# Optimization experiments

Measured on AMD Instinct MI355X. Metric: run time of the kernel, lower is better.

The kernel has to match this reference:

```python
import jax, jax.numpy as jnp
import numpy as np

B, S, D, H, E, F = 32, 196, 768, 12, 8, 3072  # batch, seq, d_model, heads, experts, ffn
DH = D // H
EPS = 1e-5


def setup_inputs() -> dict:
    key = jax.random.key(0)
    ks = jax.random.split(key, 16)
    n = lambda k, shape, s=0.02: (jax.random.normal(k, shape, dtype=jnp.float32) * s)
    return {
        "q": jax.random.normal(ks[0], (B, S, D), dtype=jnp.float32),
        "k": jax.random.normal(ks[1], (B, S, D), dtype=jnp.float32),
        "v": jax.random.normal(ks[2], (B, S, D), dtype=jnp.float32),
        "Wq": n(ks[3], (D, D)), "bq": jnp.zeros((D,), jnp.float32),
        "Wk": n(ks[4], (D, D)), "bk": jnp.zeros((D,), jnp.float32),
        "Wv": n(ks[5], (D, D)), "bv": jnp.zeros((D,), jnp.float32),
        "Wo": n(ks[6], (D, D)), "bo": jnp.zeros((D,), jnp.float32),
        "ln1_g": jnp.ones((D,), jnp.float32), "ln1_b": jnp.zeros((D,), jnp.float32),
        "ln2_g": jnp.ones((D,), jnp.float32), "ln2_b": jnp.zeros((D,), jnp.float32),
        "Wg": n(ks[7], (D, E)), "bg": jnp.zeros((E,), jnp.float32),
        "W1": n(ks[8], (E, D, F)), "b1": jnp.zeros((E, F), jnp.float32),
        "W2": n(ks[9], (E, F, D)), "b2": jnp.zeros((E, D), jnp.float32),
    }


def _layernorm(x, g, b):
    mu = jnp.mean(x, axis=-1, keepdims=True)
    var = jnp.mean(jnp.square(x - mu), axis=-1, keepdims=True)
    return (x - mu) * jax.lax.rsqrt(var + EPS) * g + b


def reference(q, k, v, Wq, bq, Wk, bk, Wv, bv, Wo, bo,
              ln1_g, ln1_b, ln2_g, ln2_b, Wg, bg, W1, b1, W2, b2):
    # --- multi-head attention (batch_first, scaled dot product) ---
    qh = (q @ Wq + bq).reshape(B, S, H, DH)
    kh = (k @ Wk + bk).reshape(B, S, H, DH)
    vh = (v @ Wv + bv).reshape(B, S, H, DH)
    scores = jnp.einsum('bqhd,bkhd->bhqk', qh, kh) / np.float32(np.sqrt(DH))
    attn = jax.nn.softmax(scores, axis=-1)
    ctx = jnp.einsum('bhqk,bkhd->bqhd', attn, vh).reshape(B, S, D)
    attn_out = ctx @ Wo + bo

    # --- residual + LN 1 ---
    x = _layernorm(q + attn_out, ln1_g, ln1_b)

    # --- MoE: per-token soft gating over per-expert FFNs ---
    gates = jax.nn.softmax(x @ Wg + bg, axis=-1)                 # [B,S,E]
    h = jax.nn.gelu(jnp.einsum('bsd,edf->bsef', x, W1) + b1,
                    approximate=False)                            # [B,S,E,F]
    y = jnp.einsum('bsef,efd->bsed', h, W2) + b2                 # [B,S,E,D]
    moe_out = jnp.einsum('bse,bsed->bsd', gates, y)              # [B,S,D]

    # --- residual + LN 2 ---
    return _layernorm(x + moe_out, ln2_g, ln2_b)
```

## Files before the change

### kernel.cpp

```cpp
#include <hip/hip_runtime.h>
#include <cmath>

#define B_  32
#define S_  196
#define D_  768
#define H_  12
#define E_  8
#define F_  3072
#define DH_ 64
#define T_  (B_ * S_)

typedef unsigned short ushort_t;
typedef short   s16x8   __attribute__((ext_vector_type(8)));
typedef __bf16  bf16x8_t __attribute__((ext_vector_type(8)));
typedef float   f32x4   __attribute__((ext_vector_type(4)));

struct ABFrag {
    unsigned int r[4];
    __device__ operator s16x8()    const { return __builtin_bit_cast(s16x8, *this); }
    __device__ operator bf16x8_t() const { return __builtin_bit_cast(bf16x8_t, *this); }
};

__device__ __forceinline__ ushort_t f2bf(float f) {
    unsigned int x = __float_as_uint(f);
    return (ushort_t)((x + 0x7fffu + ((x >> 16) & 1u)) >> 16);
}

__device__ __forceinline__ void glds16(const void* g, void* l) {
    __builtin_amdgcn_global_load_lds((const __attribute__((address_space(1))) void*)g,
                                     (__attribute__((address_space(3))) void*)l,
                                     16, 0, 0);
}

__device__ __forceinline__ void atomAddF(float* p, float v) {
    __hip_atomic_fetch_add(p, v, __ATOMIC_RELAXED, __HIP_MEMORY_SCOPE_AGENT);
}

template<int EPI>
__global__ __launch_bounds__(256)
void gemm_bt(const ushort_t* __restrict__ A0, const ushort_t* __restrict__ A1,
             const ushort_t* __restrict__ A2, const ushort_t* __restrict__ Bt,
             const float* __restrict__ bias,
             float* __restrict__ C0, float* __restrict__ C1,
             float* __restrict__ C2,
             ushort_t* __restrict__ Cb0, ushort_t* __restrict__ Cb1,
             int M, int N, int K, int lda, int ldb,
             size_t strideB, int biasStride,
             const float* __restrict__ gates, int expertBase)
{
    __shared__ ushort_t Alds[128 * 32];
    __shared__ ushort_t Blds[128 * 32];

    const int tid = threadIdx.x;
    const int w  = tid >> 6, l = tid & 63;
    const int wr = w >> 1,  wc = w & 1;
    const int rg = l >> 4,  fr = l & 15;
    const int brow = blockIdx.y * 128;
    const int bcol = blockIdx.x * 128;
    const int z    = blockIdx.z;

    int e = 0, koff = 0;
    const ushort_t* A = A0;
    const ushort_t* Bp = Bt;
    if (EPI == 1) { e = z; Bp += (size_t)e * strideB; }
    if (EPI == 2) { e = z >> 1; koff = (z & 1) * K; A = e ? A1 : A0;
                    Bp += (size_t)e * strideB; }

    const int seg = (EPI == 3) ? (bcol / 768) : 0;
    if (EPI == 3) A = (seg == 0 ? A0 : seg == 1 ? A1 : A2);
    float* Cf = (EPI == 3) ? (seg == 0 ? C0 : seg == 1 ? C1 : C2) : C0;
    const int ldc   = (EPI == 3) ? 768 : N;
    const int ccol0 = (EPI == 3) ? (bcol - seg * 768) : bcol;

    const int srow = tid >> 2;
    const int scol = (tid & 3) << 3;
    const ushort_t* gA = A  + (size_t)(brow + srow) * lda + koff + scol;
    const ushort_t* gB = Bp + (size_t)(bcol + srow) * ldb + koff + scol;
    ushort_t* lA = &Alds[w * 512];
    ushort_t* lB = &Blds[w * 512];

    f32x4 acc[4][4] = {};
    const int aoff = (wr * 64 + fr) * 32 + rg * 8;
    const int boff = (wc * 64 + fr) * 32 + rg * 8;

    for (int k0 = 0; k0 < K; k0 += 32) {
        if (k0) __syncthreads();
        glds16(gA,                    lA);
        glds16(gA + (size_t)64 * lda, lA + 2048);
        glds16(gB,                    lB);
        glds16(gB + (size_t)64 * ldb, lB + 2048);
        gA += 32; gB += 32;
        __syncthreads();

        ABFrag af[4], bfr[4];
        #pragma unroll
        for (int m = 0; m < 4; ++m) af[m]  = *(const ABFrag*)&Alds[aoff + m * 512];
        #pragma unroll
        for (int n = 0; n < 4; ++n) bfr[n] = *(const ABFrag*)&Blds[boff + n * 512];
        #pragma unroll
        for (int m = 0; m < 4; ++m)
            #pragma unroll
            for (int n = 0; n < 4; ++n)
                acc[m][n] = __builtin_amdgcn_mfma_f32_16x16x32_bf16(
                                af[m], bfr[n], acc[m][n], 0, 0, 0);
    }

    #pragma unroll
    for (int m = 0; m < 4; ++m) {
        #pragma unroll
        for (int n = 0; n < 4; ++n) {
            const int cg   = bcol  + wc * 64 + n * 16 + fr;
            const int ocol = ccol0 + wc * 64 + n * 16 + fr;
            float bv;
            if (EPI == 1)      bv = bias[e * biasStride + cg];
            else if (EPI == 2) bv = (z & 1) ? 0.f : bias[e * biasStride + cg];
            else               bv = bias[cg];
            #pragma unroll
            for (int j = 0; j < 4; ++j) {
                const int row = brow + wr * 64 + m * 16 + rg * 4 + j;
                float vv = acc[m][n][j] + bv;
                if (EPI == 1) {
                    vv = 0.5f * vv * (1.0f + erff(vv * 0.70710678118654752f));
                    (e ? Cb1 : Cb0)[(size_t)row * N + ocol] = f2bf(vv);
                } else if (EPI == 2) {
                    atomAddF(&Cf[(size_t)row * ldc + ocol],
                             gates[(size_t)row * E_ + expertBase + e] * vv);
                } else {
                    Cf[(size_t)row * ldc + ocol] = vv;
                }
            }
        }
    }
}

__global__ __launch_bounds__(256)
void convert_bf16(const float* __restrict__ in, ushort_t* __restrict__ out)
{
    const int i = blockIdx.x * 256 + threadIdx.x;
    float4 v = ((const float4*)in)[i];
    ushort4 o;
    o.x = f2bf(v.x); o.y = f2bf(v.y); o.z = f2bf(v.z); o.w = f2bf(v.w);
    ((ushort4*)out)[i] = o;
}

__global__ __launch_bounds__(256)
void transpose_to_bf16(const float* __restrict__ in, ushort_t* __restrict__ out,
                       int R, int C, size_t inStride, size_t outStride)
{
    __shared__ float tile[64][65];
    in  += (size_t)blockIdx.z * inStride;
    out += (size_t)blockIdx.z * outStride;
    const int bc = blockIdx.x * 64;
    const int br = blockIdx.y * 64;
    const int lr = threadIdx.x >> 4;
    const int lc = (threadIdx.x & 15) << 2;
    #pragma unroll
    for (int i = 0; i < 64; i += 16) {
        float4 v = *(const float4*)&in[(size_t)(br + lr + i) * C + bc + lc];
        tile[lr + i][lc + 0] = v.x; tile[lr + i][lc + 1] = v.y;
        tile[lr + i][lc + 2] = v.z; tile[lr + i][lc + 3] = v.w;
    }
    __syncthreads();
    #pragma unroll
    for (int i = 0; i < 64; i += 16) {
        const int orow = lr + i;
        ushort4 o;
        o.x = f2bf(tile[lc + 0][orow]);
        o.y = f2bf(tile[lc + 1][orow]);
        o.z = f2bf(tile[lc + 2][orow]);
        o.w = f2bf(tile[lc + 3][orow]);
        *(ushort4*)&out[(size_t)(bc + orow) * R + br + lc] = o;
    }
}

#define KB_ 28
__global__ __launch_bounds__(256)
void attn_kernel(const float* __restrict__ qh, const float* __restrict__ kh,
                 const float* __restrict__ vh, float* __restrict__ ctx)
{
    __shared__ float Ks[S_ * DH_];
    const int bh = blockIdx.x;
    const int b  = bh / H_;
    const int h  = bh % H_;
    const int tid = threadIdx.x;

    for (int i = tid; i < S_ * 16; i += 256) {
        const int s = i >> 4, d4 = i & 15;
        ((float4*)Ks)[s * 16 + d4] =
            *(const float4*)&kh[((size_t)(b * S_ + s)) * D_ + h * DH_ + d4 * 4];
    }
    __syncthreads();
    if (tid >= S_) return;

    float qf[DH_];
    const float* qrow = qh + ((size_t)(b * S_ + tid)) * D_ + h * DH_;
    #pragma unroll
    for (int d = 0; d < DH_; d += 4) {
        float4 v4 = *(const float4*)(qrow + d);
        qf[d+0] = v4.x * 0.125f; qf[d+1] = v4.y * 0.125f;
        qf[d+2] = v4.z * 0.125f; qf[d+3] = v4.w * 0.125f;
    }

    float m = -1e30f, lsum = 0.f;
    float acc[DH_] = {};
    const float* vbase = vh + ((size_t)b * S_) * D_ + h * DH_;

    for (int kc = 0; kc < S_; kc += KB_) {
        float sc[KB_];
        #pragma unroll
        for (int kk = 0; kk < KB_; ++kk) {
            const float* kr = &Ks[(kc + kk) * DH_];
            float s0 = 0.f, s1 = 0.f, s2 = 0.f, s3 = 0.f;
            #pragma unroll
            for (int d = 0; d < DH_; d += 4) {
                s0 = fmaf(qf[d+0], kr[d+0], s0);
                s1 = fmaf(qf[d+1], kr[d+1], s1);
                s2 = fmaf(qf[d+2], kr[d+2], s2);
                s3 = fmaf(qf[d+3], kr[d+3], s3);
            }
            sc[kk] = (s0 + s1) + (s2 + s3);
        }
        float cmax = sc[0];
        #pragma unroll
        for (int kk = 1; kk < KB_; ++kk) cmax = fmaxf(cmax, sc[kk]);
        const float newm  = fmaxf(m, cmax);
        const float alpha = __expf(m - newm);
        lsum *= alpha;
        #pragma unroll
        for (int d = 0; d < DH_; ++d) acc[d] *= alpha;
        m = newm;
        #pragma unroll
        for (int kk = 0; kk < KB_; ++kk) {
            sc[kk] = __expf(sc[kk] - m);
            lsum  += sc[kk];
        }
        #pragma unroll
        for (int kk = 0; kk < KB_; ++kk) {
            const float p = sc[kk];
            const float* vr = vbase + (size_t)(kc + kk) * D_;
            #pragma unroll
            for (int d = 0; d < DH_; d += 4) {
                float4 v4 = *(const float4*)(vr + d);
                acc[d+0] = fmaf(p, v4.x, acc[d+0]);
                acc[d+1] = fmaf(p, v4.y, acc[d+1]);
                acc[d+2] = fmaf(p, v4.z, acc[d+2]);
                acc[d+3] = fmaf(p, v4.w, acc[d+3]);
            }
        }
    }
    const float inv = 1.f / lsum;
    float* crow = ctx + ((size_t)(b * S_ + tid)) * D_ + h * DH_;
    #pragma unroll
    for (int d = 0; d < DH_; ++d) crow[d] = acc[d] * inv;
}

__device__ __forceinline__ float block_sum(float v, float* red)
{
    __syncthreads();
    const int lane = threadIdx.x & 63;
    const int wid  = threadIdx.x >> 6;
    #pragma unroll
    for (int off = 32; off > 0; off >>= 1) v += __shfl_down(v, off);
    if (lane == 0) red[wid] = v;
    __syncthreads();
    return red[0] + red[1] + red[2] + red[3];
}

__global__ __launch_bounds__(256)
void ln_kernel(const float* __restrict__ a, const float* __restrict__ bres,
               const float* __restrict__ g, const float* __restrict__ beta,
               float* __restrict__ out, float* __restrict__ zt)
{
    __shared__ float red[4];
    const int t   = blockIdx.x;
    const int tid = threadIdx.x;
    const float* ar = a    + (size_t)t * D_;
    const float* br = bres + (size_t)t * D_;

    float vals[3];
    float s = 0.f;
    #pragma unroll
    for (int i = 0; i < 3; ++i) {
        const int d = tid + i * 256;
        const float x = ar[d] + br[d];
        vals[i] = x;
        s += x;
        if (zt) zt[(size_t)t * D_ + d] = 0.f;
    }
    s = block_sum(s, red);
    const float mu = s * (1.f / D_);
    float qv = 0.f;
    #pragma unroll
    for (int i = 0; i < 3; ++i) { const float dv = vals[i] - mu; qv += dv * dv; }
    qv = block_sum(qv, red);
    const float rstd = rsqrtf(qv * (1.f / D_) + 1e-5f);
    #pragma unroll
    for (int i = 0; i < 3; ++i) {
        const int d = tid + i * 256;
        out[(size_t)t * D_ + d] = (vals[i] - mu) * rstd * g[d] + beta[d];
    }
}

__global__ __launch_bounds__(256)
void gate_kernel(const float* __restrict__ x, const float* __restrict__ Wg,
                 const float* __restrict__ bg, float* __restrict__ gates)
{
    const int lane = threadIdx.x & 63;
    const int wid  = threadIdx.x >> 6;
    const int t = blockIdx.x * 4 + wid;
    const float* xr = x + (size_t)t * D_;

    float accv[E_];
    #pragma unroll
    for (int e = 0; e < E_; ++e) accv[e] = 0.f;
    for (int d = lane; d < D_; d += 64) {
        const float xv = xr[d];
        const float* wr = Wg + (size_t)d * E_;
        #pragma unroll
        for (int e = 0; e < E_; ++e) accv[e] = fmaf(xv, wr[e], accv[e]);
    }
    #pragma unroll
    for (int e = 0; e < E_; ++e) {
        #pragma unroll
        for (int off = 32; off > 0; off >>= 1)
            accv[e] += __shfl_down(accv[e], off);
    }
    if (lane == 0) {
        float mx = -1e30f;
        #pragma unroll
        for (int e = 0; e < E_; ++e) { accv[e] += bg[e]; mx = fmaxf(mx, accv[e]); }
        float lsum = 0.f;
        #pragma unroll
        for (int e = 0; e < E_; ++e) { const float p = expf(accv[e] - mx); accv[e] = p; lsum += p; }
        const float inv = 1.f / lsum;
        #pragma unroll
        for (int e = 0; e < E_; ++e) gates[(size_t)t * E_ + e] = accv[e] * inv;
    }
}

__global__ void concat3_kernel(const float* __restrict__ a, const float* __restrict__ b,
                               const float* __restrict__ c, float* __restrict__ o)
{
    const int i = blockIdx.x * 256 + threadIdx.x;
    if (i < 768)       o[i] = a[i];
    else if (i < 1536) o[i] = b[i - 768];
    else if (i < 2304) o[i] = c[i - 1536];
}

extern "C" void kernel_launch(void* const* d_in, const int* in_sizes, int n_in,
                              void* d_out, int out_size, void* d_ws, size_t ws_size,
                              hipStream_t stream)
{
    const float* q    = (const float*)d_in[0];
    const float* k    = (const float*)d_in[1];
    const float* v    = (const float*)d_in[2];
    const float* Wq   = (const float*)d_in[3];
    const float* bq   = (const float*)d_in[4];
    const float* Wk   = (const float*)d_in[5];
    const float* bk   = (const float*)d_in[6];
    const float* Wv   = (const float*)d_in[7];
    const float* bv   = (const float*)d_in[8];
    const float* Wo   = (const float*)d_in[9];
    const float* bo   = (const float*)d_in[10];
    const float* ln1g = (const float*)d_in[11];
    const float* ln1b = (const float*)d_in[12];
    const float* ln2g = (const float*)d_in[13];
    const float* ln2b = (const float*)d_in[14];
    const float* Wg   = (const float*)d_in[15];
    const float* bg   = (const float*)d_in[16];
    const float* W1   = (const float*)d_in[17];
    const float* b1   = (const float*)d_in[18];
    const float* W2   = (const float*)d_in[19];
    const float* b2   = (const float*)d_in[20];
    float* out = (float*)d_out;
    float* ws  = (float*)d_ws;

    const size_t TD = (size_t)T_ * D_;
    const size_t DD = (size_t)D_ * D_;
    const size_t DF = (size_t)D_ * F_;

    float* qh      = ws;
    float* x       = ws + TD;
    float* kh      = x;
    float* vh      = ws + 2 * TD;
    float* ctx     = ws + 3 * TD;
    float* moe     = ws + 4 * TD;
    ushort_t* hb0  = (ushort_t*)(ws + 2 * TD);
    ushort_t* hb1  = (ushort_t*)(ws + 5 * TD);
    ushort_t* xb   = (ushort_t*)qh;
    float* gates   = qh + TD / 2;
    float* attnout = qh;

    ushort_t* qb   = (ushort_t*)(ws + 5 * TD);
    ushort_t* kb   = qb + TD;
    ushort_t* vb   = kb + TD;
    ushort_t* ctxb = qb;

    ushort_t* wqkvt = (ushort_t*)(ws + 7 * TD);
    ushort_t* wot   = wqkvt + 3 * DD;
    float*    bcat  = (float*)(wot + DD);
    ushort_t* w1t   = (ushort_t*)(bcat + 2304);
    ushort_t* w2t   = w1t + 2 * DF;

    const dim3 blk(256);
    const int  cgrid = (int)(TD / 1024);

    concat3_kernel<<<dim3(9), blk, 0, stream>>>(bq, bk, bv, bcat);
    transpose_to_bf16<<<dim3(D_/64, D_/64), blk, 0, stream>>>(Wq, wqkvt,          D_, D_, 0, 0);
    transpose_to_bf16<<<dim3(D_/64, D_/64), blk, 0, stream>>>(Wk, wqkvt + DD,     D_, D_, 0, 0);
    transpose_to_bf16<<<dim3(D_/64, D_/64), blk, 0, stream>>>(Wv, wqkvt + 2 * DD, D_, D_, 0, 0);
    transpose_to_bf16<<<dim3(D_/64, D_/64), blk, 0, stream>>>(Wo, wot,            D_, D_, 0, 0);

    convert_bf16<<<cgrid, blk, 0, stream>>>(q, qb);
    convert_bf16<<<cgrid, blk, 0, stream>>>(k, kb);
    convert_bf16<<<cgrid, blk, 0, stream>>>(v, vb);
    gemm_bt<3><<<dim3(18, 49), blk, 0, stream>>>(qb, kb, vb, wqkvt, bcat,
                                                 qh, kh, vh, nullptr, nullptr,
                                                 T_, 2304, D_, D_, D_, 0, 0,
                                                 nullptr, 0);

    attn_kernel<<<dim3(B_ * H_), blk, 0, stream>>>(qh, kh, vh, ctx);

    convert_bf16<<<cgrid, blk, 0, stream>>>(ctx, ctxb);
    gemm_bt<0><<<dim3(6, 49), blk, 0, stream>>>(ctxb, nullptr, nullptr, wot, bo,
                                                attnout, nullptr, nullptr, nullptr, nullptr,
                                                T_, D_, D_, D_, D_, 0, 0, nullptr, 0);
    ln_kernel<<<dim3(T_), blk, 0, stream>>>(q, attnout, ln1g, ln1b, x, moe);

    gate_kernel<<<dim3(T_ / 4), blk, 0, stream>>>(x, Wg, bg, gates);
    convert_bf16<<<cgrid, blk, 0, stream>>>(x, xb);

    for (int g = 0; g < 4; ++g) {
        const int e0 = 2 * g;
        transpose_to_bf16<<<dim3(F_/64, D_/64, 2), blk, 0, stream>>>(
            W1 + (size_t)e0 * DF, w1t, D_, F_, DF, DF);
        transpose_to_bf16<<<dim3(D_/64, F_/64, 2), blk, 0, stream>>>(
            W2 + (size_t)e0 * DF, w2t, F_, D_, DF, DF);
        gemm_bt<1><<<dim3(24, 49, 2), blk, 0, stream>>>(
            xb, nullptr, nullptr, w1t, b1 + (size_t)e0 * F_,
            nullptr, nullptr, nullptr, hb0, hb1,
            T_, F_, D_, D_, D_, DF, F_, nullptr, 0);
        gemm_bt<2><<<dim3(6, 49, 4), blk, 0, stream>>>(
            hb0, hb1, nullptr, w2t, b2 + (size_t)e0 * D_,
            moe, nullptr, nullptr, nullptr, nullptr,
            T_, D_, F_ / 2, F_, F_, DF, D_, gates, e0);
    }

    ln_kernel<<<dim3(T_), blk, 0, stream>>>(x, moe, ln2g, ln2b, out, nullptr);
}
```

Before: 1.631 ms.

## Double GEMM K-tile with swizzled LDS, split attention over keys, fuse bf16 conversions

The GEMM now stages 64-wide K tiles with an XOR-swizzled LDS layout, which halves the number of barriers per tile and is meant to reduce bank conflicts. The exact erf GELU is replaced by a tanh-based approximation. Attention is split into two key halves across twice as many blocks, followed by a combine kernel that writes bf16 context directly. LayerNorm 1 also emits the bf16 copy of x, removing two conversion kernels. The costs are extra LDS use, an extra partial-results buffer, and slight numerical deviation from the tanh GELU.

```diff
diff --git a/kernel.cpp b/kernel.cpp
--- a/kernel.cpp
+++ b/kernel.cpp
@@ -9,6 +9,7 @@
 #define F_  3072
 #define DH_ 64
 #define T_  (B_ * S_)
+#define PR_ (B_ * H_ * S_)
 
 typedef unsigned short ushort_t;
 typedef short   s16x8   __attribute__((ext_vector_type(8)));
@@ -34,6 +35,12 @@
 
 __device__ __forceinline__ void atomAddF(float* p, float v) {
     __hip_atomic_fetch_add(p, v, __ATOMIC_RELAXED, __HIP_MEMORY_SCOPE_AGENT);
+}
+
+__device__ __forceinline__ float gelu_f(float x) {
+    const float y = 0.7978845608028654f * (x + 0.044715f * x * x * x);
+    const float t = __expf(fminf(2.f * y, 80.f));
+    return 0.5f * x * (1.f + (t - 1.f) / (t + 1.f));
 }
 
 template<int EPI>
@@ -48,8 +55,8 @@
              size_t strideB, int biasStride,
              const float* __restrict__ gates, int expertBase)
 {
-    __shared__ ushort_t Alds[128 * 32];
-    __shared__ ushort_t Blds[128 * 32];
+    __shared__ ushort_t Alds[128 * 64];
+    __shared__ ushort_t Blds[128 * 64];
 
     const int tid = threadIdx.x;
     const int w  = tid >> 6, l = tid & 63;
@@ -72,37 +79,44 @@
     const int ldc   = (EPI == 3) ? 768 : N;
     const int ccol0 = (EPI == 3) ? (bcol - seg * 768) : bcol;
 
-    const int srow = tid >> 2;
-    const int scol = (tid & 3) << 3;
+    const int srow = tid >> 3;
+    const int scol = ((tid & 7) << 3) ^ ((srow & 7) << 3);
     const ushort_t* gA = A  + (size_t)(brow + srow) * lda + koff + scol;
     const ushort_t* gB = Bp + (size_t)(bcol + srow) * ldb + koff + scol;
     ushort_t* lA = &Alds[w * 512];
     ushort_t* lB = &Blds[w * 512];
 
     f32x4 acc[4][4] = {};
-    const int aoff = (wr * 64 + fr) * 32 + rg * 8;
-    const int boff = (wc * 64 + fr) * 32 + rg * 8;
-
-    for (int k0 = 0; k0 < K; k0 += 32) {
+    const int arow0 = (wr * 64 + fr) * 64;
+    const int brow0 = (wc * 64 + fr) * 64;
+
+    for (int k0 = 0; k0 < K; k0 += 64) {
         if (k0) __syncthreads();
-        glds16(gA,                    lA);
-        glds16(gA + (size_t)64 * lda, lA + 2048);
-        glds16(gB,                    lB);
-        glds16(gB + (size_t)64 * ldb, lB + 2048);
-        gA += 32; gB += 32;
+        #pragma unroll
+        for (int s = 0; s < 4; ++s) {
+            glds16(gA + (size_t)(s * 32) * lda, lA + s * 2048);
+            glds16(gB + (size_t)(s * 32) * ldb, lB + s * 2048);
+        }
+        gA += 64; gB += 64;
         __syncthreads();
 
-        ABFrag af[4], bfr[4];
-        #pragma unroll
-        for (int m = 0; m < 4; ++m) af[m]  = *(const ABFrag*)&Alds[aoff + m * 512];
-        #pragma unroll
-        for (int n = 0; n < 4; ++n) bfr[n] = *(const ABFrag*)&Blds[boff + n * 512];
-        #pragma unroll
-        for (int m = 0; m < 4; ++m)
+        #pragma unroll
+        for (int kk = 0; kk < 2; ++kk) {
+            const int xk = (((kk << 2) | rg) ^ (fr & 7)) << 3;
+            ABFrag af[4], bfr[4];
+            #pragma unroll
+            for (int m = 0; m < 4; ++m)
+                af[m]  = *(const ABFrag*)&Alds[arow0 + m * 1024 + xk];
             #pragma unroll
             for (int n = 0; n < 4; ++n)
-                acc[m][n] = __builtin_amdgcn_mfma_f32_16x16x32_bf16(
-                                af[m], bfr[n], acc[m][n], 0, 0, 0);
+                bfr[n] = *(const ABFrag*)&Blds[brow0 + n * 1024 + xk];
+            #pragma unroll
+            for (int m = 0; m < 4; ++m)
+                #pragma unroll
+                for (int n = 0; n < 4; ++n)
+                    acc[m][n] = __builtin_amdgcn_mfma_f32_16x16x32_bf16(
+                                    af[m], bfr[n], acc[m][n], 0, 0, 0);
+        }
     }
 
     #pragma unroll
@@ -120,7 +134,7 @@
                 const int row = brow + wr * 64 + m * 16 + rg * 4 + j;
                 float vv = acc[m][n][j] + bv;
                 if (EPI == 1) {
-                    vv = 0.5f * vv * (1.0f + erff(vv * 0.70710678118654752f));
+                    vv = gelu_f(vv);
                     (e ? Cb1 : Cb0)[(size_t)row * N + ocol] = f2bf(vv);
                 } else if (EPI == 2) {
                     atomAddF(&Cf[(size_t)row * ldc + ocol],
@@ -173,21 +187,25 @@
     }
 }
 
-#define KB_ 28
-__global__ __launch_bounds__(256)
-void attn_kernel(const float* __restrict__ qh, const float* __restrict__ kh,
-                 const float* __restrict__ vh, float* __restrict__ ctx)
-{
-    __shared__ float Ks[S_ * DH_];
-    const int bh = blockIdx.x;
-    const int b  = bh / H_;
-    const int h  = bh % H_;
+#define KL_  (S_ / 2)
+#define KB2_ 14
+__global__ __launch_bounds__(256)
+void attn_part(const float* __restrict__ qh, const float* __restrict__ kh,
+               const float* __restrict__ vh, float* __restrict__ part,
+               float* __restrict__ ml)
+{
+    __shared__ float Ks[KL_ * DH_];
+    const int blk = blockIdx.x;
+    const int bh  = blk >> 1;
+    const int kc  = blk & 1;
+    const int b = bh / H_, h = bh % H_;
     const int tid = threadIdx.x;
-
-    for (int i = tid; i < S_ * 16; i += 256) {
+    const int k0 = kc * KL_;
+
+    for (int i = tid; i < KL_ * 16; i += 256) {
         const int s = i >> 4, d4 = i & 15;
-        ((float4*)Ks)[s * 16 + d4] =
-            *(const float4*)&kh[((size_t)(b * S_ + s)) * D_ + h * DH_ + d4 * 4];
+        ((float4*)Ks)[i] =
+            *(const float4*)&kh[((size_t)(b * S_ + k0 + s)) * D_ + h * DH_ + d4 * 4];
     }
     __syncthreads();
     if (tid >= S_) return;
@@ -203,13 +221,13 @@
 
     float m = -1e30f, lsum = 0.f;
     float acc[DH_] = {};
-    const float* vbase = vh + ((size_t)b * S_) * D_ + h * DH_;
-
-    for (int kc = 0; kc < S_; kc += KB_) {
-        float sc[KB_];
-        #pragma unroll
-        for (int kk = 0; kk < KB_; ++kk) {
-            const float* kr = &Ks[(kc + kk) * DH_];
+    const float* vbase = vh + ((size_t)(b * S_ + k0)) * D_ + h * DH_;
+
+    for (int kch = 0; kch < KL_; kch += KB2_) {
+        float sc[KB2_];
+        #pragma unroll
+        for (int kk = 0; kk < KB2_; ++kk) {
+            const float* kr = &Ks[(kch + kk) * DH_];
             float s0 = 0.f, s1 = 0.f, s2 = 0.f, s3 = 0.f;
             #pragma unroll
             for (int d = 0; d < DH_; d += 4) {
@@ -222,7 +240,7 @@
         }
         float cmax = sc[0];
         #pragma unroll
-        for (int kk = 1; kk < KB_; ++kk) cmax = fmaxf(cmax, sc[kk]);
+        for (int kk = 1; kk < KB2_; ++kk) cmax = fmaxf(cmax, sc[kk]);
         const float newm  = fmaxf(m, cmax);
         const float alpha = __expf(m - newm);
         lsum *= alpha;
@@ -230,14 +248,14 @@
         for (int d = 0; d < DH_; ++d) acc[d] *= alpha;
         m = newm;
         #pragma unroll
-        for (int kk = 0; kk < KB_; ++kk) {
+        for (int kk = 0; kk < KB2_; ++kk) {
             sc[kk] = __expf(sc[kk] - m);
             lsum  += sc[kk];
         }
         #pragma unroll
-        for (int kk = 0; kk < KB_; ++kk) {
+        for (int kk = 0; kk < KB2_; ++kk) {
             const float p = sc[kk];
-            const float* vr = vbase + (size_t)(kc + kk) * D_;
+            const float* vr = vbase + (size_t)(kch + kk) * D_;
             #pragma unroll
             for (int d = 0; d < DH_; d += 4) {
                 float4 v4 = *(const float4*)(vr + d);
@@ -248,10 +266,32 @@
             }
         }
     }
-    const float inv = 1.f / lsum;
-    float* crow = ctx + ((size_t)(b * S_ + tid)) * D_ + h * DH_;
-    #pragma unroll
-    for (int d = 0; d < DH_; ++d) crow[d] = acc[d] * inv;
+
+    const size_t r = (size_t)kc * PR_ + (size_t)bh * S_ + tid;
+    float* pr = part + r * DH_;
+    #pragma unroll
+    for (int d = 0; d < DH_; d += 4)
+        *(float4*)(pr + d) = make_float4(acc[d], acc[d+1], acc[d+2], acc[d+3]);
+    ((float2*)ml)[r] = make_float2(m, lsum);
+}
+
+__global__ __launch_bounds__(256)
+void attn_combine(const float* __restrict__ part, const float* __restrict__ ml,
+                  ushort_t* __restrict__ ctxb)
+{
+    const size_t i   = (size_t)blockIdx.x * 256 + threadIdx.x;
+    const size_t row = i >> 6;
+    const int d = (int)(i & 63);
+    float2 ml0 = ((const float2*)ml)[row];
+    float2 ml1 = ((const float2*)ml)[PR_ + row];
+    const float M  = fmaxf(ml0.x, ml1.x);
+    const float e0 = __expf(ml0.x - M), e1 = __expf(ml1.x - M);
+    const float inv = 1.f / (e0 * ml0.y + e1 * ml1.y);
+    const float o = (e0 * part[row * 64 + d] +
+                     e1 * part[(size_t)PR_ * 64 + row * 64 + d]) * inv;
+    const int bh = (int)(row / S_), qi = (int)(row % S_);
+    const int b = bh / H_, h = bh % H_;
+    ctxb[((size_t)(b * S_ + qi)) * D_ + h * DH_ + d] = f2bf(o);
 }
 
 __device__ __forceinline__ float block_sum(float v, float* red)
@@ -269,7 +309,8 @@
 __global__ __launch_bounds__(256)
 void ln_kernel(const float* __restrict__ a, const float* __restrict__ bres,
                const float* __restrict__ g, const float* __restrict__ beta,
-               float* __restrict__ out, float* __restrict__ zt)
+               float* __restrict__ out, ushort_t* __restrict__ xbout,
+               float* __restrict__ zt)
 {
     __shared__ float red[4];
     const int t   = blockIdx.x;
@@ -297,7 +338,9 @@
     #pragma unroll
     for (int i = 0; i < 3; ++i) {
         const int d = tid + i * 256;
-        out[(size_t)t * D_ + d] = (vals[i] - mu) * rstd * g[d] + beta[d];
+        const float o = (vals[i] - mu) * rstd * g[d] + beta[d];
+        out[(size_t)t * D_ + d] = o;
+        if (xbout) xbout[(size_t)t * D_ + d] = f2bf(o);
     }
 }
 
@@ -383,24 +426,25 @@
     float* x       = ws + TD;
     float* kh      = x;
     float* vh      = ws + 2 * TD;
-    float* ctx     = ws + 3 * TD;
+    ushort_t* ctxb = (ushort_t*)(ws + 3 * TD);
+    float* ml      = ws + 4 * TD;
     float* moe     = ws + 4 * TD;
+    float* part    = ws + 5 * TD;
     ushort_t* hb0  = (ushort_t*)(ws + 2 * TD);
     ushort_t* hb1  = (ushort_t*)(ws + 5 * TD);
-    ushort_t* xb   = (ushort_t*)qh;
     float* gates   = qh + TD / 2;
     float* attnout = qh;
 
     ushort_t* qb   = (ushort_t*)(ws + 5 * TD);
     ushort_t* kb   = qb + TD;
     ushort_t* vb   = kb + TD;
-    ushort_t* ctxb = qb;
 
     ushort_t* wqkvt = (ushort_t*)(ws + 7 * TD);
     ushort_t* wot   = wqkvt + 3 * DD;
     float*    bcat  = (float*)(wot + DD);
     ushort_t* w1t   = (ushort_t*)(bcat + 2304);
     ushort_t* w2t   = w1t + 2 * DF;
+    ushort_t* xb    = w2t + 2 * DF;
 
     const dim3 blk(256);
     const int  cgrid = (int)(TD / 1024);
@@ -419,16 +463,15 @@
                                                  T_, 2304, D_, D_, D_, 0, 0,
                                                  nullptr, 0);
 
-    attn_kernel<<<dim3(B_ * H_), blk, 0, stream>>>(qh, kh, vh, ctx);
-
-    convert_bf16<<<cgrid, blk, 0, stream>>>(ctx, ctxb);
+    attn_part<<<dim3(B_ * H_ * 2), blk, 0, stream>>>(qh, kh, vh, part, ml);
+    attn_combine<<<dim3((int)(TD / 256)), blk, 0, stream>>>(part, ml, ctxb);
+
     gemm_bt<0><<<dim3(6, 49), blk, 0, stream>>>(ctxb, nullptr, nullptr, wot, bo,
                                                 attnout, nullptr, nullptr, nullptr, nullptr,
                                                 T_, D_, D_, D_, D_, 0, 0, nullptr, 0);
-    ln_kernel<<<dim3(T_), blk, 0, stream>>>(q, attnout, ln1g, ln1b, x, moe);
+    ln_kernel<<<dim3(T_), blk, 0, stream>>>(q, attnout, ln1g, ln1b, x, xb, moe);
 
     gate_kernel<<<dim3(T_ / 4), blk, 0, stream>>>(x, Wg, bg, gates);
-    convert_bf16<<<cgrid, blk, 0, stream>>>(x, xb);
 
     for (int g = 0; g < 4; ++g) {
         const int e0 = 2 * g;
@@ -446,5 +489,5 @@
             T_, D_, F_ / 2, F_, F_, DF, D_, gates, e0);
     }
 
-    ln_kernel<<<dim3(T_), blk, 0, stream>>>(x, moe, ln2g, ln2b, out, nullptr);
-}
+    ln_kernel<<<dim3(T_), blk, 0, stream>>>(x, moe, ln2g, ln2b, out, nullptr, nullptr);
+}
```

Result: faster. 1.452 ms (-11.0%).
